# Kernel tuning notes

Measured on AMD Instinct MI355X. Metric: run time of the kernel, lower is better.

The kernel has to match this reference:

```python
import jax, jax.numpy as jnp
import numpy as np

N = 100_000      # nodes
E = 1_600_000    # edges (avg degree 16)
D_IN = 256
D_OUT = 128


def setup_inputs() -> dict:
    key = jax.random.key(0)
    ks = jax.random.split(key, 13)
    stdv = 1.0 / np.sqrt(D_OUT)      # matches reset_parameters
    std_att = 1.0                    # att_vec_* have fan 1 -> stdv 1
    std_av = 1.0 / np.sqrt(3.0)
    return {
        "x": jax.random.normal(ks[0], (N, D_IN), dtype=jnp.float32),
        "edge_src": jax.random.randint(ks[1], (E,), 0, N),
        "edge_dst": jax.random.randint(ks[2], (E,), 0, N),
        "w_low": jax.random.uniform(ks[3], (E,), dtype=jnp.float32) / 16.0,   # ~normalized adj
        "w_high": jax.random.normal(ks[4], (E,), dtype=jnp.float32) / 16.0,    # high-pass weights can be +/-
        "w_unnorm": jax.random.uniform(ks[5], (E,), dtype=jnp.float32),
        "W_low": jax.random.uniform(ks[6], (D_IN, D_OUT), jnp.float32, -stdv, stdv),
        "W_high": jax.random.uniform(ks[7], (D_IN, D_OUT), jnp.float32, -stdv, stdv),
        "W_mlp": jax.random.uniform(ks[8], (D_IN, D_OUT), jnp.float32, -stdv, stdv),
        "a_low": jax.random.uniform(ks[9], (D_OUT, 1), jnp.float32, -std_att, std_att),
        "a_high": jax.random.uniform(ks[10], (D_OUT, 1), jnp.float32, -std_att, std_att),
        "a_mlp": jax.random.uniform(ks[11], (D_OUT, 1), jnp.float32, -std_att, std_att),
        "att_vec": jax.random.uniform(ks[12], (3, 3), jnp.float32, -std_av, std_av),
    }


def _spmm(w, src, dst, h, n):
    # sparse [n,n] @ dense [n,d]: gather source rows, weight, scatter-add to dest
    return jax.ops.segment_sum(w[:, None] * h[src], dst, num_segments=n)


def reference(x, edge_src, edge_dst, w_low, w_high, w_unnorm,
              W_low, W_high, W_mlp, a_low, a_high, a_mlp, att_vec):
    n = x.shape[0]
    # variant=False path: relu(spmm(adj, x @ W))
    h_low = jax.nn.relu(_spmm(w_low, edge_src, edge_dst, x @ W_low, n))
    h_high = jax.nn.relu(_spmm(w_high, edge_src, edge_dst, x @ W_high, n))
    h_mlp = jax.nn.relu(x @ W_mlp)
    # attention3: sigmoid of per-branch scalar scores -> 3x3 mix -> softmax (T=3)
    scores = jnp.concatenate([h_low @ a_low, h_high @ a_high, h_mlp @ a_mlp], axis=1)  # [n,3]
    att = jax.nn.softmax((jax.nn.sigmoid(scores) @ att_vec) / 3.0, axis=1)
    return 3.0 * (att[:, 0:1] * h_low + att[:, 1:2] * h_high + att[:, 2:3] * h_mlp)
```

## Files before the change

kernel.cpp:

```cpp
#include <hip/hip_runtime.h>
#include <hip/hip_bf16.h>
#include <math.h>

#define D_IN   256
#define D_OUT  128
#define DZ     384
#define NHB    256

typedef __attribute__((ext_vector_type(8))) short short8;
typedef __attribute__((ext_vector_type(4))) float floatx4;

__device__ __forceinline__ unsigned short f2bf(float f) {
  union { float f; unsigned u; } v; v.f = f;
  unsigned r = v.u + 0x7fffu + ((v.u >> 16) & 1u);
  return (unsigned short)(r >> 16);
}

__global__ __launch_bounds__(256) void hist_prep_kernel(
    const float* __restrict__ Wl, const float* __restrict__ Wh,
    const float* __restrict__ Wm, unsigned short* __restrict__ Bpack,
    const float* __restrict__ x, unsigned short* __restrict__ xb, int n8,
    const int* __restrict__ dst, int* __restrict__ bh, int E, int NB1) {
  __shared__ int hist[1024];
  const int bid = blockIdx.x;
  const int t = threadIdx.x;
  if (bid < NHB) {
    for (int k = t; k < NB1; k += 256) hist[k] = 0;
    __syncthreads();
    const int chunk = (E + NHB - 1) / NHB;
    const int base = bid * chunk;
    const int lim = min(E, base + chunk);
    for (int e = base + t; e < lim; e += 256) atomicAdd(&hist[dst[e] >> 7], 1);
    __syncthreads();
    for (int k = t; k < NB1; k += 256) bh[k * NHB + bid] = hist[k];
  } else if (bid < NHB + 384) {
    int tt = (bid - NHB) * 256 + t;
    int j = tt & 7;
    int lane = (tt >> 3) & 63;
    int f = tt >> 9;
    int nt = f % 24, kt = f / 24;
    int k = kt * 32 + (lane >> 4) * 8 + j;
    int n_ = nt * 16 + (lane & 15);
    const float* W = (n_ < 128) ? Wl : (n_ < 256 ? Wh : Wm);
    Bpack[tt] = f2bf(W[k * D_OUT + (n_ & 127)]);
  } else {
    int i = (bid - NHB - 384) * 256 + t;
    if (i < n8) {
      const float4* p = (const float4*)x + (size_t)i * 2;
      float4 f0 = p[0], f1 = p[1];
      short8 o;
      o[0] = (short)f2bf(f0.x); o[1] = (short)f2bf(f0.y);
      o[2] = (short)f2bf(f0.z); o[3] = (short)f2bf(f0.w);
      o[4] = (short)f2bf(f1.x); o[5] = (short)f2bf(f1.y);
      o[6] = (short)f2bf(f1.z); o[7] = (short)f2bf(f1.w);
      ((short8*)xb)[i] = o;
    }
  }
}

__global__ __launch_bounds__(256) void scan1_kernel(
    const int* __restrict__ cnt, int* __restrict__ outp,
    int* __restrict__ bsum, int n) {
  __shared__ int sd[256];
  int t = threadIdx.x;
  int base = blockIdx.x * 1024 + t * 4;
  int v0 = base + 0 < n ? cnt[base + 0] : 0;
  int v1 = base + 1 < n ? cnt[base + 1] : 0;
  int v2 = base + 2 < n ? cnt[base + 2] : 0;
  int v3 = base + 3 < n ? cnt[base + 3] : 0;
  int tsum = v0 + v1 + v2 + v3;
  sd[t] = tsum;
  __syncthreads();
  for (int off = 1; off < 256; off <<= 1) {
    int add = (t >= off) ? sd[t - off] : 0;
    __syncthreads();
    sd[t] += add;
    __syncthreads();
  }
  int excl = sd[t] - tsum;
  if (base + 0 < n) outp[base + 0] = excl;
  if (base + 1 < n) outp[base + 1] = excl + v0;
  if (base + 2 < n) outp[base + 2] = excl + v0 + v1;
  if (base + 3 < n) outp[base + 3] = excl + v0 + v1 + v2;
  if (t == 255) bsum[blockIdx.x] = sd[255];
}

__global__ __launch_bounds__(256) void scan2_kernel(int* __restrict__ bsum,
                                                    int nb) {
  __shared__ int sd[256];
  int t = threadIdx.x;
  int v = t < nb ? bsum[t] : 0;
  sd[t] = v;
  __syncthreads();
  for (int off = 1; off < 256; off <<= 1) {
    int add = (t >= off) ? sd[t - off] : 0;
    __syncthreads();
    sd[t] += add;
    __syncthreads();
  }
  if (t < nb) bsum[t] = sd[t] - v;
}

__global__ void scan3_kernel(int* __restrict__ outp,
                             const int* __restrict__ bsum, int n) {
  int i = blockIdx.x * 256 + threadIdx.x;
  if (i < n) outp[i] += bsum[i >> 10];
}

#define LDSROW 392
__global__ __launch_bounds__(512, 4) void gemm_sort_kernel(
    const unsigned short* __restrict__ xb,
    const unsigned short* __restrict__ Bpack, unsigned short* __restrict__ Z,
    int n_nodes, const int* __restrict__ src, const int* __restrict__ dst,
    const float* __restrict__ wlo, const float* __restrict__ whi,
    const int* __restrict__ bhscan, uint2* __restrict__ tmp, int E, int NB1) {
  __shared__ unsigned short tile[64 * LDSROW];
  const int bid = blockIdx.x;

  int gemm_id;
  if (bid < 2 * NHB) {
    if ((bid & 1) == 0) {
      int rb = bid >> 1;
      int* cur = (int*)tile;
      int t = threadIdx.x;
      for (int k = t; k < NB1; k += 512) cur[k] = bhscan[k * NHB + rb];
      __syncthreads();
      const int chunk = (E + NHB - 1) / NHB;
      const int base = rb * chunk;
      const int lim = min(E, base + chunk);
      for (int e = base + t; e < lim; e += 512) {
        int d = dst[e];
        int pos = atomicAdd(&cur[d >> 7], 1);
        unsigned wl = f2bf(wlo[e]), wh = f2bf(whi[e]);
        tmp[pos] = make_uint2((unsigned)src[e] | ((unsigned)(d & 127) << 20),
                              wl | (wh << 16));
      }
      return;
    }
    gemm_id = bid >> 1;
  } else {
    gemm_id = bid - 2 * NHB + NHB;
  }

  const int lane = threadIdx.x & 63;
  const int w = threadIdx.x >> 6;
  const int rowbase = gemm_id * 64;
  const int m16 = lane & 15, quad = lane >> 4;

  floatx4 acc[4][3];
#pragma unroll
  for (int s = 0; s < 4; s++)
#pragma unroll
    for (int c = 0; c < 3; c++) acc[s][c] = (floatx4)(0.f);

  const short8* xr[4];
#pragma unroll
  for (int s = 0; s < 4; s++) {
    int r = rowbase + s * 16 + m16;
    if (r > n_nodes - 1) r = n_nodes - 1;
    xr[s] = (const short8*)xb + (size_t)r * 32 + quad;
  }
  const short8* bp = (const short8*)Bpack + lane;

#pragma unroll
  for (int kt = 0; kt < 8; kt++) {
    short8 a[4];
#pragma unroll
    for (int s = 0; s < 4; s++) a[s] = xr[s][kt * 4];
#pragma unroll
    for (int c = 0; c < 3; c++) {
      short8 b = bp[(kt * 24 + w * 3 + c) * 64];
#pragma unroll
      for (int s = 0; s < 4; s++)
        acc[s][c] =
            __builtin_amdgcn_mfma_f32_16x16x32_bf16(a[s], b, acc[s][c], 0, 0, 0);
    }
  }

#pragma unroll
  for (int s = 0; s < 4; s++)
#pragma unroll
    for (int c = 0; c < 3; c++)
#pragma unroll
      for (int r = 0; r < 4; r++)
        tile[(s * 16 + quad * 4 + r) * LDSROW + (w * 3 + c) * 16 + m16] =
            f2bf(acc[s][c][r]);
  __syncthreads();

#pragma unroll
  for (int it = 0; it < 6; it++) {
    int chunk = it * 512 + threadIdx.x;
    int row = chunk / 48, col = (chunk % 48) * 8;
    int grow = rowbase + row;
    if (grow < n_nodes)
      *(short8*)(Z + (size_t)grow * DZ + col) =
          *(const short8*)&tile[row * LDSROW + col];
  }
}

__global__ __launch_bounds__(256) void fine_kernel(
    const uint2* __restrict__ tmp, const int* __restrict__ bhscan,
    uint2* __restrict__ meta, int* __restrict__ rowptr, int NB1, int n, int E) {
  __shared__ int fh[128];
  __shared__ int sd[128];
  __shared__ int cur[128];
  const int b = blockIdx.x;
  const int t = threadIdx.x;
  const int s0 = bhscan[b * NHB];
  const int s1 = (b == NB1 - 1) ? E : bhscan[(b + 1) * NHB];

  if (t < 128) fh[t] = 0;
  __syncthreads();
  for (int i = s0 + t; i < s1; i += 256)
    atomicAdd(&fh[(tmp[i].x >> 20) & 127], 1);
  __syncthreads();

  if (t < 128) sd[t] = fh[t];
  __syncthreads();
  for (int off = 1; off < 128; off <<= 1) {
    int add = (t >= off && t < 128) ? sd[t - off] : 0;
    __syncthreads();
    if (t < 128) sd[t] += add;
    __syncthreads();
  }
  if (t < 128) {
    int excl = sd[t] - fh[t];
    cur[t] = excl;
    int node = b * 128 + t;
    if (node < n) rowptr[node] = s0 + excl;
  }
  if (b == 0 && t == 0) rowptr[n] = E;
  __syncthreads();

  for (int i = s0 + t; i < s1; i += 256) {
    uint2 v = tmp[i];
    int d = (v.x >> 20) & 127;
    int pos = s0 + atomicAdd(&cur[d], 1);
    meta[pos] = make_uint2(v.x & 0xFFFFFu, v.y);
  }
}

__global__ __launch_bounds__(128) void node_kernel(
    const unsigned short* __restrict__ Zh, const int* __restrict__ rowptr,
    const uint2* __restrict__ meta, const float* __restrict__ a_low,
    const float* __restrict__ a_high, const float* __restrict__ a_mlp,
    const float* __restrict__ att_vec, float* __restrict__ out, int n_nodes) {
  int node = blockIdx.x * 2 + (threadIdx.x >> 6);
  if (node >= n_nodes) return;
  node = __builtin_amdgcn_readfirstlane(node);
  const int lane = threadIdx.x & 63;
  const int isHigh = lane >> 5;
  const int dbase = (lane & 31) * 4;
  const char* Zb = (const char*)Zh;

  const int start = rowptr[node];
  const int end = rowptr[node + 1];

  float acc0 = 0.f, acc1 = 0.f, acc2 = 0.f, acc3 = 0.f;
  auto wsel = [&](unsigned p) {
    return __uint_as_float(isHigh ? (p & 0xffff0000u) : (p << 16));
  };
  auto step = [&](uint2 z, float wv) {
    acc0 += wv * __uint_as_float(z.x << 16);
    acc1 += wv * __uint_as_float(z.x & 0xffff0000u);
    acc2 += wv * __uint_as_float(z.y << 16);
    acc3 += wv * __uint_as_float(z.y & 0xffff0000u);
  };

  int j = start;
  const int nfull = (end - start) & ~7;
  for (; j < start + nfull; j += 8) {
    uint2 m[8], z[8];
#pragma unroll
    for (int u = 0; u < 8; u++) m[u] = meta[j + u];
#pragma unroll
    for (int u = 0; u < 8; u++)
      z[u] = *(const uint2*)(Zb + (size_t)m[u].x * 768 + lane * 8);
#pragma unroll
    for (int u = 0; u < 8; u++) step(z[u], wsel(m[u].y));
  }
  for (; j < end; j++) {
    uint2 m0 = meta[j];
    uint2 z0 = *(const uint2*)(Zb + (size_t)m0.x * 768 + lane * 8);
    step(z0, wsel(m0.y));
  }

  float h0 = fmaxf(acc0, 0.f), h1 = fmaxf(acc1, 0.f);
  float h2 = fmaxf(acc2, 0.f), h3 = fmaxf(acc3, 0.f);

  uint2 zm =
      *(const uint2*)(Zb + (size_t)node * 768 + 512 + (size_t)(lane & 31) * 8);
  float q0 = fmaxf(__uint_as_float(zm.x << 16), 0.f);
  float q1 = fmaxf(__uint_as_float(zm.x & 0xffff0000u), 0.f);
  float q2 = fmaxf(__uint_as_float(zm.y << 16), 0.f);
  float q3 = fmaxf(__uint_as_float(zm.y & 0xffff0000u), 0.f);

  const float* av_b = isHigh ? a_high : a_low;
  float4 ab = *(const float4*)&av_b[dbase];
  float4 am = *(const float4*)&a_mlp[dbase];
  float v1 = h0 * ab.x + h1 * ab.y + h2 * ab.z + h3 * ab.w;
  float v2 = isHigh ? 0.f : (q0 * am.x + q1 * am.y + q2 * am.z + q3 * am.w);
#pragma unroll
  for (int off = 1; off < 32; off <<= 1) {
    v1 += __shfl_xor(v1, off);
    v2 += __shfl_xor(v2, off);
  }
  float s_lo = __shfl(v1, 0);
  float s_hi = __shfl(v1, 32);
  float s_ml = __shfl(v2, 0);

  float g0 = 1.f / (1.f + __expf(-s_lo));
  float g1 = 1.f / (1.f + __expf(-s_hi));
  float g2 = 1.f / (1.f + __expf(-s_ml));
  const float inv3 = 1.f / 3.f;
  float m0 = (g0 * att_vec[0] + g1 * att_vec[3] + g2 * att_vec[6]) * inv3;
  float m1 = (g0 * att_vec[1] + g1 * att_vec[4] + g2 * att_vec[7]) * inv3;
  float m2 = (g0 * att_vec[2] + g1 * att_vec[5] + g2 * att_vec[8]) * inv3;
  float mx = fmaxf(m0, fmaxf(m1, m2));
  float e0 = __expf(m0 - mx), e1 = __expf(m1 - mx), e2 = __expf(m2 - mx);
  float inv = 1.f / (e0 + e1 + e2);
  float c0 = 3.f * inv * e0, c1 = 3.f * inv * e1, c2 = 3.f * inv * e2;

  float hh0 = __shfl_xor(h0, 32);
  float hh1 = __shfl_xor(h1, 32);
  float hh2 = __shfl_xor(h2, 32);
  float hh3 = __shfl_xor(h3, 32);

  if (!isHigh) {
    float4 o;
    o.x = c0 * h0 + c1 * hh0 + c2 * q0;
    o.y = c0 * h1 + c1 * hh1 + c2 * q1;
    o.z = c0 * h2 + c1 * hh2 + c2 * q2;
    o.w = c0 * h3 + c1 * hh3 + c2 * q3;
    *(float4*)&out[(size_t)node * D_OUT + dbase] = o;
  }
}

extern "C" void kernel_launch(void* const* d_in, const int* in_sizes, int n_in,
                              void* d_out, int out_size, void* d_ws,
                              size_t ws_size, hipStream_t stream) {
  const float* x    = (const float*)d_in[0];
  const int*   esrc = (const int*)d_in[1];
  const int*   edst = (const int*)d_in[2];
  const float* wlo  = (const float*)d_in[3];
  const float* whi  = (const float*)d_in[4];
  const float* Wl   = (const float*)d_in[6];
  const float* Wh   = (const float*)d_in[7];
  const float* Wm   = (const float*)d_in[8];
  const float* alo  = (const float*)d_in[9];
  const float* ahi  = (const float*)d_in[10];
  const float* amlp = (const float*)d_in[11];
  const float* av   = (const float*)d_in[12];
  float* out = (float*)d_out;

  const int N = in_sizes[0] / D_IN;
  const int E = in_sizes[1];
  const int NB1 = (N + 127) >> 7;
  const int M = NB1 * NHB;

  char* ws = (char*)d_ws;
  size_t off = 0;
  auto carve = [&](size_t bytes) -> void* {
    void* p = ws + off;
    off = (off + bytes + 255) & ~(size_t)255;
    return p;
  };
  unsigned short* Z      = (unsigned short*)carve((size_t)N * DZ * 2);
  unsigned short* xb     = (unsigned short*)carve((size_t)N * D_IN * 2);
  unsigned short* Bpack  = (unsigned short*)carve(98304 * 2);
  int*   bh     = (int*)carve((size_t)M * 4);
  int*   bhscan = (int*)carve((size_t)M * 4);
  int*   bsum   = (int*)carve(256 * 4);
  int*   rowptr = (int*)carve((size_t)(N + 1) * 4);
  uint2* tmp    = (uint2*)carve((size_t)E * 8);
  uint2* meta   = (uint2*)carve((size_t)E * 8);

  int n8 = in_sizes[0] / 8;
  int nxb = (n8 + 255) / 256;

  hist_prep_kernel<<<NHB + 384 + nxb, 256, 0, stream>>>(Wl, Wh, Wm, Bpack, x,
                                                        xb, n8, edst, bh, E,
                                                        NB1);
  int nb1s = (M + 1023) / 1024;
  scan1_kernel<<<nb1s, 256, 0, stream>>>(bh, bhscan, bsum, M);
  scan2_kernel<<<1, 256, 0, stream>>>(bsum, nb1s);
  scan3_kernel<<<(M + 255) / 256, 256, 0, stream>>>(bhscan, bsum, M);

  int ngemm = (N + 63) / 64;
  gemm_sort_kernel<<<ngemm + NHB, 512, 0, stream>>>(
      xb, Bpack, Z, N, esrc, edst, wlo, whi, bhscan, tmp, E, NB1);

  fine_kernel<<<NB1, 256, 0, stream>>>(tmp, bhscan, meta, rowptr, NB1, N, E);

  node_kernel<<<(N + 1) / 2, 128, 0, stream>>>(Z, rowptr, meta, alo, ahi, amlp,
                                               av, out, N);
}
```

Measured before the change: 451.2 us.

## Fuse fine sort into node kernel via LDS bucket sort and fold scan3

Removes the scan3 kernel by adding the block-sum offset wherever scan results are read. Also removes the fine_kernel and its global meta/rowptr arrays: each 512-thread node block now counting-sorts its 128-node coarse bucket into shared memory and then aggregates per node from LDS. Buckets larger than CAP take a slow fallback path in which every wave rescans the overflow edges in global memory. With only NB1 (~782) blocks of 512 threads and about 37KB of LDS each, the node phase has less parallelism and occupancy than the old 50k small blocks.

New measurement: 487.5 us. 8.1% more time.

```diff
diff --git a/kernel.cpp b/kernel.cpp
--- a/kernel.cpp
+++ b/kernel.cpp
@@ -6,6 +6,7 @@
 #define D_OUT  128
 #define DZ     384
 #define NHB    256
+#define CAP    4608
 
 typedef __attribute__((ext_vector_type(8))) short short8;
 typedef __attribute__((ext_vector_type(4))) float floatx4;
@@ -101,19 +102,14 @@
   if (t < nb) bsum[t] = sd[t] - v;
 }
 
-__global__ void scan3_kernel(int* __restrict__ outp,
-                             const int* __restrict__ bsum, int n) {
-  int i = blockIdx.x * 256 + threadIdx.x;
-  if (i < n) outp[i] += bsum[i >> 10];
-}
-
 #define LDSROW 392
 __global__ __launch_bounds__(512, 4) void gemm_sort_kernel(
     const unsigned short* __restrict__ xb,
     const unsigned short* __restrict__ Bpack, unsigned short* __restrict__ Z,
     int n_nodes, const int* __restrict__ src, const int* __restrict__ dst,
     const float* __restrict__ wlo, const float* __restrict__ whi,
-    const int* __restrict__ bhscan, uint2* __restrict__ tmp, int E, int NB1) {
+    const int* __restrict__ bhscan, const int* __restrict__ bsum,
+    uint2* __restrict__ tmp, int E, int NB1) {
   __shared__ unsigned short tile[64 * LDSROW];
   const int bid = blockIdx.x;
 
@@ -123,7 +119,10 @@
       int rb = bid >> 1;
       int* cur = (int*)tile;
       int t = threadIdx.x;
-      for (int k = t; k < NB1; k += 512) cur[k] = bhscan[k * NHB + rb];
+      for (int k = t; k < NB1; k += 512) {
+        int idx = k * NHB + rb;
+        cur[k] = bhscan[idx] + bsum[idx >> 10];
+      }
       __syncthreads();
       const int chunk = (E + NHB - 1) / NHB;
       const int base = rb * chunk;
@@ -198,141 +197,149 @@
   }
 }
 
-__global__ __launch_bounds__(256) void fine_kernel(
-    const uint2* __restrict__ tmp, const int* __restrict__ bhscan,
-    uint2* __restrict__ meta, int* __restrict__ rowptr, int NB1, int n, int E) {
-  __shared__ int fh[128];
-  __shared__ int sd[128];
-  __shared__ int cur[128];
+__global__ __launch_bounds__(512) void node_kernel(
+    const unsigned short* __restrict__ Zh, const uint2* __restrict__ tmp,
+    const int* __restrict__ bhscan, const int* __restrict__ bsum,
+    const float* __restrict__ a_low, const float* __restrict__ a_high,
+    const float* __restrict__ a_mlp, const float* __restrict__ att_vec,
+    float* __restrict__ out, int NB1, int n_nodes, int E) {
+  __shared__ uint2 smeta[CAP];
+  __shared__ int fh[128], sd[128], cur[128], nstart[129];
   const int b = blockIdx.x;
   const int t = threadIdx.x;
-  const int s0 = bhscan[b * NHB];
-  const int s1 = (b == NB1 - 1) ? E : bhscan[(b + 1) * NHB];
+  const char* Zb = (const char*)Zh;
+
+  auto scanidx = [&](int i) { return bhscan[i] + bsum[i >> 10]; };
+  const int s0 = scanidx(b * NHB);
+  const int segEnd = (b == NB1 - 1) ? E : scanidx((b + 1) * NHB);
+  int cnt = segEnd - s0;
+  if (cnt > CAP) cnt = CAP;
 
   if (t < 128) fh[t] = 0;
   __syncthreads();
-  for (int i = s0 + t; i < s1; i += 256)
-    atomicAdd(&fh[(tmp[i].x >> 20) & 127], 1);
-  __syncthreads();
-
+  for (int i = t; i < cnt; i += 512) atomicAdd(&fh[(tmp[s0 + i].x >> 20) & 127], 1);
+  __syncthreads();
   if (t < 128) sd[t] = fh[t];
   __syncthreads();
   for (int off = 1; off < 128; off <<= 1) {
-    int add = (t >= off && t < 128) ? sd[t - off] : 0;
+    int add = (t < 128 && t >= off) ? sd[t - off] : 0;
     __syncthreads();
     if (t < 128) sd[t] += add;
     __syncthreads();
   }
   if (t < 128) {
-    int excl = sd[t] - fh[t];
-    cur[t] = excl;
-    int node = b * 128 + t;
-    if (node < n) rowptr[node] = s0 + excl;
-  }
-  if (b == 0 && t == 0) rowptr[n] = E;
-  __syncthreads();
-
-  for (int i = s0 + t; i < s1; i += 256) {
-    uint2 v = tmp[i];
+    nstart[t] = sd[t] - fh[t];
+    cur[t] = sd[t] - fh[t];
+  }
+  if (t == 0) nstart[128] = cnt;
+  __syncthreads();
+  for (int i = t; i < cnt; i += 512) {
+    uint2 v = tmp[s0 + i];
     int d = (v.x >> 20) & 127;
-    int pos = s0 + atomicAdd(&cur[d], 1);
-    meta[pos] = make_uint2(v.x & 0xFFFFFu, v.y);
-  }
-}
-
-__global__ __launch_bounds__(128) void node_kernel(
-    const unsigned short* __restrict__ Zh, const int* __restrict__ rowptr,
-    const uint2* __restrict__ meta, const float* __restrict__ a_low,
-    const float* __restrict__ a_high, const float* __restrict__ a_mlp,
-    const float* __restrict__ att_vec, float* __restrict__ out, int n_nodes) {
-  int node = blockIdx.x * 2 + (threadIdx.x >> 6);
-  if (node >= n_nodes) return;
-  node = __builtin_amdgcn_readfirstlane(node);
-  const int lane = threadIdx.x & 63;
+    int pos = atomicAdd(&cur[d], 1);
+    smeta[pos] = make_uint2(v.x & 0xFFFFFu, v.y);
+  }
+  __syncthreads();
+
+  const int wv = t >> 6;
+  const int lane = t & 63;
   const int isHigh = lane >> 5;
   const int dbase = (lane & 31) * 4;
-  const char* Zb = (const char*)Zh;
-
-  const int start = rowptr[node];
-  const int end = rowptr[node + 1];
-
-  float acc0 = 0.f, acc1 = 0.f, acc2 = 0.f, acc3 = 0.f;
+
   auto wsel = [&](unsigned p) {
     return __uint_as_float(isHigh ? (p & 0xffff0000u) : (p << 16));
   };
-  auto step = [&](uint2 z, float wv) {
-    acc0 += wv * __uint_as_float(z.x << 16);
-    acc1 += wv * __uint_as_float(z.x & 0xffff0000u);
-    acc2 += wv * __uint_as_float(z.y << 16);
-    acc3 += wv * __uint_as_float(z.y & 0xffff0000u);
-  };
-
-  int j = start;
-  const int nfull = (end - start) & ~7;
-  for (; j < start + nfull; j += 8) {
-    uint2 m[8], z[8];
-#pragma unroll
-    for (int u = 0; u < 8; u++) m[u] = meta[j + u];
-#pragma unroll
-    for (int u = 0; u < 8; u++)
-      z[u] = *(const uint2*)(Zb + (size_t)m[u].x * 768 + lane * 8);
-#pragma unroll
-    for (int u = 0; u < 8; u++) step(z[u], wsel(m[u].y));
-  }
-  for (; j < end; j++) {
-    uint2 m0 = meta[j];
-    uint2 z0 = *(const uint2*)(Zb + (size_t)m0.x * 768 + lane * 8);
-    step(z0, wsel(m0.y));
-  }
-
-  float h0 = fmaxf(acc0, 0.f), h1 = fmaxf(acc1, 0.f);
-  float h2 = fmaxf(acc2, 0.f), h3 = fmaxf(acc3, 0.f);
-
-  uint2 zm =
-      *(const uint2*)(Zb + (size_t)node * 768 + 512 + (size_t)(lane & 31) * 8);
-  float q0 = fmaxf(__uint_as_float(zm.x << 16), 0.f);
-  float q1 = fmaxf(__uint_as_float(zm.x & 0xffff0000u), 0.f);
-  float q2 = fmaxf(__uint_as_float(zm.y << 16), 0.f);
-  float q3 = fmaxf(__uint_as_float(zm.y & 0xffff0000u), 0.f);
-
-  const float* av_b = isHigh ? a_high : a_low;
-  float4 ab = *(const float4*)&av_b[dbase];
-  float4 am = *(const float4*)&a_mlp[dbase];
-  float v1 = h0 * ab.x + h1 * ab.y + h2 * ab.z + h3 * ab.w;
-  float v2 = isHigh ? 0.f : (q0 * am.x + q1 * am.y + q2 * am.z + q3 * am.w);
-#pragma unroll
-  for (int off = 1; off < 32; off <<= 1) {
-    v1 += __shfl_xor(v1, off);
-    v2 += __shfl_xor(v2, off);
-  }
-  float s_lo = __shfl(v1, 0);
-  float s_hi = __shfl(v1, 32);
-  float s_ml = __shfl(v2, 0);
-
-  float g0 = 1.f / (1.f + __expf(-s_lo));
-  float g1 = 1.f / (1.f + __expf(-s_hi));
-  float g2 = 1.f / (1.f + __expf(-s_ml));
-  const float inv3 = 1.f / 3.f;
-  float m0 = (g0 * att_vec[0] + g1 * att_vec[3] + g2 * att_vec[6]) * inv3;
-  float m1 = (g0 * att_vec[1] + g1 * att_vec[4] + g2 * att_vec[7]) * inv3;
-  float m2 = (g0 * att_vec[2] + g1 * att_vec[5] + g2 * att_vec[8]) * inv3;
-  float mx = fmaxf(m0, fmaxf(m1, m2));
-  float e0 = __expf(m0 - mx), e1 = __expf(m1 - mx), e2 = __expf(m2 - mx);
-  float inv = 1.f / (e0 + e1 + e2);
-  float c0 = 3.f * inv * e0, c1 = 3.f * inv * e1, c2 = 3.f * inv * e2;
-
-  float hh0 = __shfl_xor(h0, 32);
-  float hh1 = __shfl_xor(h1, 32);
-  float hh2 = __shfl_xor(h2, 32);
-  float hh3 = __shfl_xor(h3, 32);
-
-  if (!isHigh) {
-    float4 o;
-    o.x = c0 * h0 + c1 * hh0 + c2 * q0;
-    o.y = c0 * h1 + c1 * hh1 + c2 * q1;
-    o.z = c0 * h2 + c1 * hh2 + c2 * q2;
-    o.w = c0 * h3 + c1 * hh3 + c2 * q3;
-    *(float4*)&out[(size_t)node * D_OUT + dbase] = o;
+
+  for (int ni = wv; ni < 128; ni += 8) {
+    int node = b * 128 + ni;
+    if (node >= n_nodes) continue;
+    node = __builtin_amdgcn_readfirstlane(node);
+
+    const int start = nstart[ni];
+    const int end = nstart[ni + 1];
+
+    float acc0 = 0.f, acc1 = 0.f, acc2 = 0.f, acc3 = 0.f;
+    auto step = [&](uint2 z, float wv_) {
+      acc0 += wv_ * __uint_as_float(z.x << 16);
+      acc1 += wv_ * __uint_as_float(z.x & 0xffff0000u);
+      acc2 += wv_ * __uint_as_float(z.y << 16);
+      acc3 += wv_ * __uint_as_float(z.y & 0xffff0000u);
+    };
+
+    int j = start;
+    const int nfull = (end - start) & ~7;
+    for (; j < start + nfull; j += 8) {
+      uint2 m[8], z[8];
+#pragma unroll
+      for (int u = 0; u < 8; u++) m[u] = smeta[j + u];
+#pragma unroll
+      for (int u = 0; u < 8; u++)
+        z[u] = *(const uint2*)(Zb + (size_t)m[u].x * 768 + lane * 8);
+#pragma unroll
+      for (int u = 0; u < 8; u++) step(z[u], wsel(m[u].y));
+    }
+    for (; j < end; j++) {
+      uint2 m0 = smeta[j];
+      uint2 z0 = *(const uint2*)(Zb + (size_t)m0.x * 768 + lane * 8);
+      step(z0, wsel(m0.y));
+    }
+    for (int i = s0 + CAP; i < segEnd; i++) {
+      uint2 v = tmp[i];
+      if ((int)((v.x >> 20) & 127) == ni) {
+        uint2 z0 = *(const uint2*)(Zb + (size_t)(v.x & 0xFFFFFu) * 768 + lane * 8);
+        step(z0, wsel(v.y));
+      }
+    }
+
+    float h0 = fmaxf(acc0, 0.f), h1 = fmaxf(acc1, 0.f);
+    float h2 = fmaxf(acc2, 0.f), h3 = fmaxf(acc3, 0.f);
+
+    uint2 zm =
+        *(const uint2*)(Zb + (size_t)node * 768 + 512 + (size_t)(lane & 31) * 8);
+    float q0 = fmaxf(__uint_as_float(zm.x << 16), 0.f);
+    float q1 = fmaxf(__uint_as_float(zm.x & 0xffff0000u), 0.f);
+    float q2 = fmaxf(__uint_as_float(zm.y << 16), 0.f);
+    float q3 = fmaxf(__uint_as_float(zm.y & 0xffff0000u), 0.f);
+
+    const float* av_b = isHigh ? a_high : a_low;
+    float4 ab = *(const float4*)&av_b[dbase];
+    float4 am = *(const float4*)&a_mlp[dbase];
+    float v1 = h0 * ab.x + h1 * ab.y + h2 * ab.z + h3 * ab.w;
+    float v2 = isHigh ? 0.f : (q0 * am.x + q1 * am.y + q2 * am.z + q3 * am.w);
+#pragma unroll
+    for (int off = 1; off < 32; off <<= 1) {
+      v1 += __shfl_xor(v1, off);
+      v2 += __shfl_xor(v2, off);
+    }
+    float s_lo = __shfl(v1, 0);
+    float s_hi = __shfl(v1, 32);
+    float s_ml = __shfl(v2, 0);
+
+    float g0 = 1.f / (1.f + __expf(-s_lo));
+    float g1 = 1.f / (1.f + __expf(-s_hi));
+    float g2 = 1.f / (1.f + __expf(-s_ml));
+    const float inv3 = 1.f / 3.f;
+    float m0 = (g0 * att_vec[0] + g1 * att_vec[3] + g2 * att_vec[6]) * inv3;
+    float m1 = (g0 * att_vec[1] + g1 * att_vec[4] + g2 * att_vec[7]) * inv3;
+    float m2 = (g0 * att_vec[2] + g1 * att_vec[5] + g2 * att_vec[8]) * inv3;
+    float mx = fmaxf(m0, fmaxf(m1, m2));
+    float e0 = __expf(m0 - mx), e1 = __expf(m1 - mx), e2 = __expf(m2 - mx);
+    float inv = 1.f / (e0 + e1 + e2);
+    float c0 = 3.f * inv * e0, c1 = 3.f * inv * e1, c2 = 3.f * inv * e2;
+
+    float hh0 = __shfl_xor(h0, 32);
+    float hh1 = __shfl_xor(h1, 32);
+    float hh2 = __shfl_xor(h2, 32);
+    float hh3 = __shfl_xor(h3, 32);
+
+    if (!isHigh) {
+      float4 o;
+      o.x = c0 * h0 + c1 * hh0 + c2 * q0;
+      o.y = c0 * h1 + c1 * hh1 + c2 * q1;
+      o.z = c0 * h2 + c1 * hh2 + c2 * q2;
+      o.w = c0 * h3 + c1 * hh3 + c2 * q3;
+      *(float4*)&out[(size_t)node * D_OUT + dbase] = o;
+    }
   }
 }
 
@@ -371,9 +378,7 @@
   int*   bh     = (int*)carve((size_t)M * 4);
   int*   bhscan = (int*)carve((size_t)M * 4);
   int*   bsum   = (int*)carve(256 * 4);
-  int*   rowptr = (int*)carve((size_t)(N + 1) * 4);
   uint2* tmp    = (uint2*)carve((size_t)E * 8);
-  uint2* meta   = (uint2*)carve((size_t)E * 8);
 
   int n8 = in_sizes[0] / 8;
   int nxb = (n8 + 255) / 256;
@@ -384,14 +389,11 @@
   int nb1s = (M + 1023) / 1024;
   scan1_kernel<<<nb1s, 256, 0, stream>>>(bh, bhscan, bsum, M);
   scan2_kernel<<<1, 256, 0, stream>>>(bsum, nb1s);
-  scan3_kernel<<<(M + 255) / 256, 256, 0, stream>>>(bhscan, bsum, M);
 
   int ngemm = (N + 63) / 64;
   gemm_sort_kernel<<<ngemm + NHB, 512, 0, stream>>>(
-      xb, Bpack, Z, N, esrc, edst, wlo, whi, bhscan, tmp, E, NB1);
-
-  fine_kernel<<<NB1, 256, 0, stream>>>(tmp, bhscan, meta, rowptr, NB1, N, E);
-
-  node_kernel<<<(N + 1) / 2, 128, 0, stream>>>(Z, rowptr, meta, alo, ahi, amlp,
-                                               av, out, N);
-}
+      xb, Bpack, Z, N, esrc, edst, wlo, whi, bhscan, bsum, tmp, E, NB1);
+
+  node_kernel<<<NB1, 512, 0, stream>>>(Z, tmp, bhscan, bsum, alo, ahi, amlp,
+                                       av, out, NB1, N, E);
+}
```
